# Kernel tuning notes

Hardware: AMD Instinct MI355X
Metric: run time of the kernel (lower is better)

The kernel has to match this reference:

```python
import jax, jax.numpy as jnp
import numpy as np

HIDDEN = 128
VOCAB = 100000
NUM_CLASSES = 5
N_LEAVES = 65536  # complete binary tree -> 2*N_LEAVES-1 = 131071 nodes


def setup_inputs() -> dict:
    key = jax.random.key(0)
    ks = jax.random.split(key, 24)
    H, C = HIDDEN, NUM_CLASSES

    def w(k, o, i):
        return (jax.random.normal(k, (o, i), jnp.float32) / np.sqrt(i)).astype(jnp.float32)

    def b(k, o):
        return jax.random.normal(k, (o,), jnp.float32) * 0.01

    inp = {
        "leaf_tokens": jax.random.randint(ks[0], (N_LEAVES,), 0, VOCAB, dtype=jnp.int64 if jax.config.jax_enable_x64 else jnp.int32).astype(jnp.int32),
        "node_labels": jax.random.randint(ks[1], (2 * N_LEAVES - 1,), 0, NUM_CLASSES).astype(jnp.int32),
        "embed": jax.random.uniform(ks[2], (VOCAB, H), jnp.float32, -0.5 / H, 0.5 / H),
        "W_i_w": w(ks[3], H, H), "W_i_b": b(ks[4], H),
        "W_o_w": w(ks[5], H, H), "W_o_b": b(ks[6], H),
        "W_u_w": w(ks[7], H, H), "W_u_b": b(ks[8], H),
        "U_i_w": w(ks[9], H, 2 * H), "U_i_b": b(ks[10], H),
        "U_o_w": w(ks[11], H, 2 * H), "U_o_b": b(ks[12], H),
        "U_u_w": w(ks[13], H, 2 * H), "U_u_b": b(ks[14], H),
        "F1_w": w(ks[15], H, H), "F1_b": b(ks[16], H),
        "F2_w": w(ks[17], H, H), "F2_b": b(ks[18], H),
        "out_w": w(ks[19], C, H), "out_b": b(ks[20], C),
    }
    return inp


def reference(leaf_tokens, node_labels, embed,
              W_i_w, W_i_b, W_o_w, W_o_b, W_u_w, W_u_b,
              U_i_w, U_i_b, U_o_w, U_o_b, U_u_w, U_u_b,
              F1_w, F1_b, F2_w, F2_b, out_w, out_b):
    def aff(x, wgt, bias):
        return x @ wgt.T + bias

    # ---- leaves: x = embed[token]; c = sigmoid(W_i x) * tanh(W_u x) ----
    x = embed[leaf_tokens]                          # [L, H]
    i = jax.nn.sigmoid(aff(x, W_i_w, W_i_b))
    o = jax.nn.sigmoid(aff(x, W_o_w, W_o_b))
    u = jnp.tanh(aff(x, W_u_w, W_u_b))
    c = i * u
    h = o * jnp.tanh(c)
    outs = [aff(h, out_w, out_b)]                   # dropout is identity at eval

    # ---- internal levels, bottom-up, all same-depth nodes batched ----
    n_levels = int(np.log2(N_LEAVES))
    for _ in range(n_levels):
        hl, hr = h[0::2], h[1::2]                   # [n/2, H] each
        cl, cr = c[0::2], c[1::2]
        xc = jnp.concatenate([hl, hr], axis=1)      # [n/2, 2H]
        i = jax.nn.sigmoid(aff(xc, U_i_w, U_i_b))
        o = jax.nn.sigmoid(aff(xc, U_o_w, U_o_b))
        u = jnp.tanh(aff(xc, U_u_w, U_u_b))
        f1 = jax.nn.sigmoid(aff(hl, F1_w, F1_b))
        f2 = jax.nn.sigmoid(aff(hr, F2_w, F2_b))
        c = i * u + f1 * cl + f2 * cr
        h = o * jnp.tanh(c)
        outs.append(aff(h, out_w, out_b))

    outputs = jnp.concatenate(outs, axis=0)         # [2L-1, num_classes]
    return outputs, node_labels
```

## Files before the change

### kernel.cpp

```cpp
#include <hip/hip_runtime.h>
#include <hip/hip_bf16.h>
#include <math.h>

#define H    128
#define NC   5
#define LPI  264
#define LPL  136
#define HPAD 136
#define CBP  132

typedef unsigned short ushort_t;
using frag_ab = __attribute__((ext_vector_type(8))) short;
using frag_cd = __attribute__((ext_vector_type(4))) float;

__device__ __forceinline__ float fsig(float x) {
    return __builtin_amdgcn_rcpf(1.0f + __expf(-x));
}
__device__ __forceinline__ float ftanh_(float x) {
    float e = __expf(-2.0f * fabsf(x));
    float t = (1.0f - e) * __builtin_amdgcn_rcpf(1.0f + e);
    return copysignf(t, x);
}
__device__ __forceinline__ ushort_t f2bf(float f) {
    __hip_bfloat16 b = __float2bfloat16(f);
    return *reinterpret_cast<ushort_t*>(&b);
}

__global__ __launch_bounds__(256) void prep_weights(
    const float* __restrict__ Ui, const float* __restrict__ Uo, const float* __restrict__ Uu,
    const float* __restrict__ F1, const float* __restrict__ F2,
    const float* __restrict__ Wi, const float* __restrict__ Wo, const float* __restrict__ Wu,
    const float* __restrict__ Wout,
    ushort_t* __restrict__ Wf, ushort_t* __restrict__ Wlf, ushort_t* __restrict__ Woutf)
{
    int e = blockIdx.x * 256 + threadIdx.x;
    if (e < 131072) {
        int kc = e >> 12, rem = e & 4095;
        int n = rem >> 3, j7 = rem & 7;
        int k = kc * 8 + j7;
        int g = n >> 7, jc = n & 127;
        float v;
        if (g == 0)      v = Ui[jc * 256 + k];
        else if (g == 1) v = Uo[jc * 256 + k];
        else if (g == 2) v = Uu[jc * 256 + k];
        else             v = (k < 128) ? F1[jc * 128 + k] : F2[jc * 128 + k - 128];
        Wf[e] = f2bf(v);
    } else if (e < 180224) {
        int e2 = e - 131072;
        int kc = e2 / 3072, rem = e2 % 3072;
        int n = rem >> 3, j7 = rem & 7;
        int k = kc * 8 + j7;
        int g = n >> 7, jc = n & 127;
        float v = (g == 0) ? Wi[jc * 128 + k] : (g == 1) ? Wo[jc * 128 + k] : Wu[jc * 128 + k];
        Wlf[e2] = f2bf(v);
    } else {
        int e3 = e - 180224;
        int kcq = e3 >> 7, rem = e3 & 127;
        int col = rem >> 3, j7 = rem & 7;
        int k = kcq * 8 + j7;
        float v = (col < NC) ? Wout[col * H + k] : 0.0f;
        Woutf[e3] = f2bf(v);
    }
}

__global__ __launch_bounds__(512) void leaf_l1_mfma(
    const int* __restrict__ tokens, const float* __restrict__ embed,
    const ushort_t* __restrict__ Wlf, const ushort_t* __restrict__ Wf,
    const ushort_t* __restrict__ Woutf,
    const float* __restrict__ bi, const float* __restrict__ bo, const float* __restrict__ bu,
    const float* __restrict__ bui, const float* __restrict__ buo, const float* __restrict__ buu,
    const float* __restrict__ bf1, const float* __restrict__ bf2,
    const float* __restrict__ bout,
    const int* __restrict__ labels, float* __restrict__ lab_out,
    ushort_t* __restrict__ h1_out, float* __restrict__ c1_out,
    float* __restrict__ out_leaf, float* __restrict__ out_l1)
{
    __shared__ ushort_t xs [32 * LPL];
    __shared__ ushort_t hh [32 * HPAD];
    __shared__ ushort_t hh2[16 * HPAD];
    __shared__ float    cbL[32 * CBP];
    __shared__ ushort_t xs2[16 * LPI];
    const int tid = threadIdx.x;
    const int node_base  = blockIdx.x * 32;
    const int node1_base = blockIdx.x * 16;

    if (tid < 64) {
        int id = blockIdx.x * 64 + tid;
        if (id < 131071) lab_out[id] = (float)labels[id];
    }

    {
        int m = tid >> 4, kp = (tid & 15) * 8;
        const float* src = embed + (size_t)tokens[node_base + m] * H + kp;
        ushort_t tmp[8];
#pragma unroll
        for (int v = 0; v < 2; ++v) {
            float4 f = *(const float4*)(src + v * 4);
            tmp[v * 4 + 0] = f2bf(f.x); tmp[v * 4 + 1] = f2bf(f.y);
            tmp[v * 4 + 2] = f2bf(f.z); tmp[v * 4 + 3] = f2bf(f.w);
        }
        *(uint4*)&xs[m * LPL + kp] = *(uint4*)tmp;
    }

    const int w = tid >> 6, lane = tid & 63;
    const int mA = lane & 15, q = lane >> 4, nlane = lane & 15;

    frag_ab wb[4];
#pragma unroll
    for (int kc8 = 0; kc8 < 4; ++kc8)
        wb[kc8] = *(const frag_ab*)&Woutf[(((kc8 * 4 + q) * 16) + nlane) * 8];
    float bout_l = (nlane < NC) ? bout[nlane] : 0.0f;

    const int jt = w;
    const int j = jt * 16 + nlane;
    __syncthreads();

    frag_ab a[2][4];
#pragma unroll
    for (int t = 0; t < 2; ++t)
#pragma unroll
        for (int kc8 = 0; kc8 < 4; ++kc8)
            a[t][kc8] = *(const frag_ab*)&xs[(t * 16 + mA) * LPL + (kc8 * 4 + q) * 8];

    {
        frag_cd acc[3][2];
#pragma unroll
        for (int g = 0; g < 3; ++g)
#pragma unroll
            for (int t = 0; t < 2; ++t) acc[g][t] = (frag_cd){0.f, 0.f, 0.f, 0.f};
#pragma unroll
        for (int kc8 = 0; kc8 < 4; ++kc8) {
            int kcq = kc8 * 4 + q;
            const ushort_t* wp = &Wlf[((size_t)kcq * 384 + jt * 16 + nlane) * 8];
#pragma unroll
            for (int g = 0; g < 3; ++g) {
                frag_ab b = *(const frag_ab*)(wp + (size_t)g * H * 8);
                acc[g][0] = __builtin_amdgcn_mfma_f32_16x16x32_bf16(a[0][kc8], b, acc[g][0], 0, 0, 0);
                acc[g][1] = __builtin_amdgcn_mfma_f32_16x16x32_bf16(a[1][kc8], b, acc[g][1], 0, 0, 0);
            }
        }
        float bi_ = bi[j], bo_ = bo[j], bu_ = bu[j];
#pragma unroll
        for (int t = 0; t < 2; ++t)
#pragma unroll
            for (int r = 0; r < 4; ++r) {
                int nloc = t * 16 + q * 4 + r;
                float i_ = fsig(acc[0][t][r] + bi_);
                float o_ = fsig(acc[1][t][r] + bo_);
                float u_ = ftanh_(acc[2][t][r] + bu_);
                float c_ = i_ * u_;
                float h_ = o_ * ftanh_(c_);
                cbL[nloc * CBP + j] = c_;
                ushort_t hb = f2bf(h_);
                hh[nloc * HPAD + j] = hb;
                xs2[(nloc >> 1) * LPI + (nloc & 1) * H + j] = hb;
            }
    }
    __syncthreads();

    frag_ab a1[8];
#pragma unroll
    for (int kc8 = 0; kc8 < 8; ++kc8)
        a1[kc8] = *(const frag_ab*)&xs2[mA * LPI + (kc8 * 4 + q) * 8];

    if (w < 2) {
        frag_cd ha = (frag_cd){0.f, 0.f, 0.f, 0.f};
#pragma unroll
        for (int kc8 = 0; kc8 < 4; ++kc8) {
            frag_ab av = *(const frag_ab*)&hh[(w * 16 + mA) * HPAD + (kc8 * 4 + q) * 8];
            ha = __builtin_amdgcn_mfma_f32_16x16x32_bf16(av, wb[kc8], ha, 0, 0, 0);
        }
        if (nlane < NC) {
#pragma unroll
            for (int r = 0; r < 4; ++r)
                out_leaf[(size_t)(node_base + w * 16 + q * 4 + r) * NC + nlane] = ha[r] + bout_l;
        }
    }

    {
        frag_cd acc[5];
#pragma unroll
        for (int g = 0; g < 5; ++g) acc[g] = (frag_cd){0.f, 0.f, 0.f, 0.f};
#pragma unroll
        for (int kc8 = 0; kc8 < 8; ++kc8) {
            int kcq = kc8 * 4 + q;
            const ushort_t* wp = &Wf[((size_t)kcq * 512 + jt * 16 + nlane) * 8];
#pragma unroll
            for (int g = 0; g < 4; ++g) {
                frag_ab b = *(const frag_ab*)(wp + (size_t)g * H * 8);
                int gi = (g < 3) ? g : (kc8 < 4 ? 3 : 4);
                acc[gi] = __builtin_amdgcn_mfma_f32_16x16x32_bf16(a1[kc8], b, acc[gi], 0, 0, 0);
            }
        }
        float bi_ = bui[j], bo_ = buo[j], bu_ = buu[j], b1_ = bf1[j], b2_ = bf2[j];
#pragma unroll
        for (int r = 0; r < 4; ++r) {
            int nloc = q * 4 + r;
            int nd = node1_base + nloc;
            float i_  = fsig(acc[0][r] + bi_);
            float o_  = fsig(acc[1][r] + bo_);
            float u_  = ftanh_(acc[2][r] + bu_);
            float f1_ = fsig(acc[3][r] + b1_);
            float f2_ = fsig(acc[4][r] + b2_);
            float cl = cbL[(2 * nloc) * CBP + j];
            float cr = cbL[(2 * nloc + 1) * CBP + j];
            float c_ = fmaf(i_, u_, fmaf(f1_, cl, f2_ * cr));
            float h_ = o_ * ftanh_(c_);
            c1_out[(size_t)nd * H + j] = c_;
            ushort_t hb = f2bf(h_);
            h1_out[(size_t)nd * H + j] = hb;
            hh2[nloc * HPAD + j] = hb;
        }
    }
    __syncthreads();

    if (w == 0) {
        frag_cd ha = (frag_cd){0.f, 0.f, 0.f, 0.f};
#pragma unroll
        for (int kc8 = 0; kc8 < 4; ++kc8) {
            frag_ab av = *(const frag_ab*)&hh2[mA * HPAD + (kc8 * 4 + q) * 8];
            ha = __builtin_amdgcn_mfma_f32_16x16x32_bf16(av, wb[kc8], ha, 0, 0, 0);
        }
        if (nlane < NC) {
#pragma unroll
            for (int r = 0; r < 4; ++r)
                out_l1[(size_t)(node1_base + q * 4 + r) * NC + nlane] = ha[r] + bout_l;
        }
    }
}

__global__ __launch_bounds__(512) void subtree_mfma(
    const ushort_t* __restrict__ h_prev, const float* __restrict__ c_prev,
    const ushort_t* __restrict__ Wf, const ushort_t* __restrict__ Woutf,
    const float* __restrict__ bui, const float* __restrict__ buo, const float* __restrict__ buu,
    const float* __restrict__ bf1, const float* __restrict__ bf2,
    const float* __restrict__ bout,
    ushort_t* __restrict__ h_out, float* __restrict__ c_out,
    float* __restrict__ out_base)
{
    __shared__ ushort_t xsA[32 * LPI];
    __shared__ ushort_t xsB[16 * LPI];
    __shared__ float    cbA[32 * CBP];
    __shared__ float    cbB[16 * CBP];
    __shared__ ushort_t hh [32 * HPAD];
    const int tid = threadIdx.x;
    const int NB  = gridDim.x;

    {
        int m = tid >> 4, kp = (tid & 15) * 16;
        const uint4* s = (const uint4*)(h_prev +
            ((size_t)2 * (blockIdx.x * 32 + m) + (kp >> 7)) * H + (kp & 127));
        uint4* d = (uint4*)&xsA[m * LPI + kp];
        d[0] = s[0]; d[1] = s[1];
    }

    const int w = tid >> 6, lane = tid & 63;
    const int mA = lane & 15, q = lane >> 4, nlane = lane & 15;

    frag_ab wb[4];
#pragma unroll
    for (int kc8 = 0; kc8 < 4; ++kc8)
        wb[kc8] = *(const frag_ab*)&Woutf[(((kc8 * 4 + q) * 16) + nlane) * 8];
    float bout_l = (nlane < NC) ? bout[nlane] : 0.0f;

    const int jt = w;
    const int j = jt * 16 + nlane;
    const float bi_ = bui[j], bo_ = buo[j], bu_ = buu[j], b1_ = bf1[j], b2_ = bf2[j];

    size_t out_off = 0;
    for (int lev = 0; lev < 4; ++lev) {
        const int N = 32 >> lev;
        const int ntiles = (N + 15) >> 4;
        const int gbase = blockIdx.x * N;
        ushort_t* xs_cur = (lev & 1) ? xsB : xsA;
        ushort_t* xs_nxt = (lev & 1) ? xsA : xsB;
        float*    cb_out = (lev & 1) ? cbB : cbA;
        const float* cb_in = (lev & 1) ? cbA : cbB;
        __syncthreads();

        for (int t = 0; t < ntiles; ++t) {
            frag_cd acc[5];
#pragma unroll
            for (int g = 0; g < 5; ++g) acc[g] = (frag_cd){0.f, 0.f, 0.f, 0.f};
#pragma unroll
            for (int kc8 = 0; kc8 < 8; ++kc8) {
                int kcq = kc8 * 4 + q;
                frag_ab av = *(const frag_ab*)&xs_cur[(t * 16 + mA) * LPI + kcq * 8];
                const ushort_t* wp = &Wf[((size_t)kcq * 512 + jt * 16 + nlane) * 8];
#pragma unroll
                for (int g = 0; g < 4; ++g) {
                    frag_ab b = *(const frag_ab*)(wp + (size_t)g * H * 8);
                    int gi = (g < 3) ? g : (kc8 < 4 ? 3 : 4);
                    acc[gi] = __builtin_amdgcn_mfma_f32_16x16x32_bf16(av, b, acc[gi], 0, 0, 0);
                }
            }
#pragma unroll
            for (int r = 0; r < 4; ++r) {
                int nloc = t * 16 + q * 4 + r;
                if (nloc < N) {
                    float i_  = fsig(acc[0][r] + bi_);
                    float o_  = fsig(acc[1][r] + bo_);
                    float u_  = ftanh_(acc[2][r] + bu_);
                    float f1_ = fsig(acc[3][r] + b1_);
                    float f2_ = fsig(acc[4][r] + b2_);
                    float cl, cr;
                    if (lev == 0) {
                        cl = c_prev[((size_t)2 * (gbase + nloc)) * H + j];
                        cr = c_prev[((size_t)2 * (gbase + nloc) + 1) * H + j];
                    } else {
                        cl = cb_in[(2 * nloc) * CBP + j];
                        cr = cb_in[(2 * nloc + 1) * CBP + j];
                    }
                    float c_ = fmaf(i_, u_, fmaf(f1_, cl, f2_ * cr));
                    float h_ = o_ * ftanh_(c_);
                    ushort_t hb = f2bf(h_);
                    hh[nloc * HPAD + j] = hb;
                    if (lev < 3) {
                        cb_out[nloc * CBP + j] = c_;
                        xs_nxt[(nloc >> 1) * LPI + (nloc & 1) * H + j] = hb;
                    } else {
                        c_out[(size_t)(gbase + nloc) * H + j] = c_;
                        h_out[(size_t)(gbase + nloc) * H + j] = hb;
                    }
                }
            }
        }
        __syncthreads();
        if (w < ntiles) {
            frag_cd ha = (frag_cd){0.f, 0.f, 0.f, 0.f};
#pragma unroll
            for (int kc8 = 0; kc8 < 4; ++kc8) {
                frag_ab av = *(const frag_ab*)&hh[(w * 16 + mA) * HPAD + (kc8 * 4 + q) * 8];
                ha = __builtin_amdgcn_mfma_f32_16x16x32_bf16(av, wb[kc8], ha, 0, 0, 0);
            }
            if (nlane < NC) {
#pragma unroll
                for (int r = 0; r < 4; ++r) {
                    int nd = w * 16 + q * 4 + r;
                    if (nd < N)
                        out_base[out_off + (size_t)(gbase + nd) * NC + nlane] = ha[r] + bout_l;
                }
            }
        }
        out_off += (size_t)NB * N * NC;
    }
}

__global__ __launch_bounds__(512) void tail_mfma(
    const ushort_t* __restrict__ h_prev, const float* __restrict__ c_prev,
    const ushort_t* __restrict__ Wf, const ushort_t* __restrict__ Woutf,
    const float* __restrict__ bui, const float* __restrict__ buo, const float* __restrict__ buu,
    const float* __restrict__ bf1, const float* __restrict__ bf2,
    const float* __restrict__ bout, float* __restrict__ out)
{
    __shared__ ushort_t xsA[64 * LPI];
    __shared__ ushort_t xsB[32 * LPI];
    __shared__ float    cbA[64 * H];
    __shared__ float    cbB[32 * H];
    __shared__ ushort_t hh[64 * HPAD];
    const int tid = threadIdx.x;
    const int w = tid >> 6, lane = tid & 63;
    const int mA = lane & 15, q = lane >> 4, nlane = lane & 15;

    {
        int m = tid >> 3, kp = (tid & 7) * 32;
        const uint4* s = (const uint4*)(h_prev + ((size_t)2 * m + (kp >> 7)) * H + (kp & 127));
        uint4* d = (uint4*)&xsA[m * LPI + kp];
#pragma unroll
        for (int i = 0; i < 4; ++i) d[i] = s[i];
    }

    frag_ab wb[4];
#pragma unroll
    for (int kc8 = 0; kc8 < 4; ++kc8)
        wb[kc8] = *(const frag_ab*)&Woutf[(((kc8 * 4 + q) * 16) + nlane) * 8];
    float bout_l = (nlane < NC) ? bout[nlane] : 0.0f;

    const int jt = w;
    const int j = jt * 16 + nlane;
    const float bi_ = bui[j], bo_ = buo[j], bu_ = buu[j], b1_ = bf1[j], b2_ = bf2[j];

    float* outp = out;
    for (int lev = 0; lev < 7; ++lev) {
        const int N = 64 >> lev;
        const int ntiles = (N + 15) >> 4;
        ushort_t* xs_cur = (lev & 1) ? xsB : xsA;
        ushort_t* xs_nxt = (lev & 1) ? xsA : xsB;
        float*    cb_out = (lev & 1) ? cbB : cbA;
        const float* cb_in = (lev & 1) ? cbA : cbB;
        __syncthreads();

        for (int t = 0; t < ntiles; ++t) {
            frag_cd acc[5];
#pragma unroll
            for (int g = 0; g < 5; ++g) acc[g] = (frag_cd){0.f, 0.f, 0.f, 0.f};
#pragma unroll
            for (int kc8 = 0; kc8 < 8; ++kc8) {
                int kcq = kc8 * 4 + q;
                frag_ab av = *(const frag_ab*)&xs_cur[(t * 16 + mA) * LPI + kcq * 8];
                const ushort_t* wp = &Wf[((size_t)kcq * 512 + jt * 16 + nlane) * 8];
#pragma unroll
                for (int g = 0; g < 4; ++g) {
                    frag_ab b = *(const frag_ab*)(wp + (size_t)g * H * 8);
                    int gi = (g < 3) ? g : (kc8 < 4 ? 3 : 4);
                    acc[gi] = __builtin_amdgcn_mfma_f32_16x16x32_bf16(av, b, acc[gi], 0, 0, 0);
                }
            }
#pragma unroll
            for (int r = 0; r < 4; ++r) {
                int nloc = t * 16 + q * 4 + r;
                if (nloc < N) {
                    float i_  = fsig(acc[0][r] + bi_);
                    float o_  = fsig(acc[1][r] + bo_);
                    float u_  = ftanh_(acc[2][r] + bu_);
                    float f1_ = fsig(acc[3][r] + b1_);
                    float f2_ = fsig(acc[4][r] + b2_);
                    float cl, cr;
                    if (lev == 0) {
                        cl = c_prev[((size_t)2 * nloc) * H + j];
                        cr = c_prev[((size_t)2 * nloc + 1) * H + j];
                    } else {
                        cl = cb_in[(2 * nloc) * H + j];
                        cr = cb_in[(2 * nloc + 1) * H + j];
                    }
                    float c_ = fmaf(i_, u_, fmaf(f1_, cl, f2_ * cr));
                    float h_ = o_ * ftanh_(c_);
                    cb_out[nloc * H + j] = c_;
                    ushort_t hb = f2bf(h_);
                    hh[nloc * HPAD + j] = hb;
                    xs_nxt[(nloc >> 1) * LPI + (nloc & 1) * H + j] = hb;
                }
            }
        }
        __syncthreads();
        if (w < ntiles) {
            frag_cd ha = (frag_cd){0.f, 0.f, 0.f, 0.f};
#pragma unroll
            for (int kc8 = 0; kc8 < 4; ++kc8) {
                frag_ab av = *(const frag_ab*)&hh[(w * 16 + mA) * HPAD + (kc8 * 4 + q) * 8];
                ha = __builtin_amdgcn_mfma_f32_16x16x32_bf16(av, wb[kc8], ha, 0, 0, 0);
            }
            if (nlane < NC) {
#pragma unroll
                for (int r = 0; r < 4; ++r) {
                    int nd = w * 16 + q * 4 + r;
                    if (nd < N) outp[(size_t)nd * NC + nlane] = ha[r] + bout_l;
                }
            }
        }
        outp += (size_t)N * NC;
    }
}

extern "C" void kernel_launch(void* const* d_in, const int* in_sizes, int n_in,
                              void* d_out, int out_size, void* d_ws, size_t ws_size,
                              hipStream_t stream)
{
    const int*   tokens = (const int*)d_in[0];
    const int*   labels = (const int*)d_in[1];
    const float* embed  = (const float*)d_in[2];
    const float* Wi = (const float*)d_in[3];  const float* bi  = (const float*)d_in[4];
    const float* Wo = (const float*)d_in[5];  const float* bo  = (const float*)d_in[6];
    const float* Wu = (const float*)d_in[7];  const float* bu  = (const float*)d_in[8];
    const float* Ui = (const float*)d_in[9];  const float* bui = (const float*)d_in[10];
    const float* Uo = (const float*)d_in[11]; const float* buo = (const float*)d_in[12];
    const float* Uu = (const float*)d_in[13]; const float* buu = (const float*)d_in[14];
    const float* F1 = (const float*)d_in[15]; const float* bf1 = (const float*)d_in[16];
    const float* F2 = (const float*)d_in[17]; const float* bf2 = (const float*)d_in[18];
    const float* Wout = (const float*)d_in[19]; const float* bout = (const float*)d_in[20];
    float* out = (float*)d_out;

    const int NL = 65536;
    char* base = (char*)d_ws;
    ushort_t* Wf    = (ushort_t*)(base);
    ushort_t* Wlf   = (ushort_t*)(base + 327680);
    ushort_t* Woutf = (ushort_t*)(base + 425984);
    ushort_t* hA    = (ushort_t*)(base + 430080);
    ushort_t* hB    = (ushort_t*)(base + 17207296);
    float*    cA    = (float*)   (base + 25595904);
    float*    cB    = (float*)   (base + 59150336);

    prep_weights<<<712, 256, 0, stream>>>(Ui, Uo, Uu, F1, F2, Wi, Wo, Wu, Wout,
                                          Wf, Wlf, Woutf);

    const size_t totalN = 2 * (size_t)NL - 1;
    float* lab_out = out + totalN * NC;

    leaf_l1_mfma<<<NL / 32, 512, 0, stream>>>(
        tokens, embed, Wlf, Wf, Woutf, bi, bo, bu, bui, buo, buu, bf1, bf2,
        bout, labels, lab_out, hB, cB, out, out + (size_t)NL * NC);

    size_t off = (size_t)(NL + NL / 2) * NC;

    subtree_mfma<<<512, 512, 0, stream>>>(
        hB, cB, Wf, Woutf, bui, buo, buu, bf1, bf2, bout, hA, cA, out + off);
    off += (size_t)(16384 + 8192 + 4096 + 2048) * NC;

    subtree_mfma<<<32, 512, 0, stream>>>(
        hA, cA, Wf, Woutf, bui, buo, buu, bf1, bf2, bout, hB, cB, out + off);
    off += (size_t)(1024 + 512 + 256 + 128) * NC;

    tail_mfma<<<1, 512, 0, stream>>>(hB, cB, Wf, Woutf, bui, buo, buu, bf1, bf2,
                                     bout, out + off);
}
```

Measured before the change: 228.7 us.

## Shrink subtree blocks to 16 rows and shift levels from tail kernel

The subtree kernel now handles 16 nodes per block instead of 32, and is templated on level count. The first launch uses twice as many blocks (1024) and the second covers five levels with 64 blocks, so the single-block tail kernel starts from 32 nodes and runs six levels instead of seven. The aim is more parallelism in the mid-tree kernels and less serial work in the one-block tail. The cost is that the subtree kernels now do much of their per-level compute with partially filled 16-row MFMA tiles.

```diff
diff --git a/kernel.cpp b/kernel.cpp
--- a/kernel.cpp
+++ b/kernel.cpp
@@ -229,7 +229,8 @@
     }
 }
 
-__global__ __launch_bounds__(512) void subtree_mfma(
+template<int LEVELS>
+__global__ __launch_bounds__(512) void subtree16_mfma(
     const ushort_t* __restrict__ h_prev, const float* __restrict__ c_prev,
     const ushort_t* __restrict__ Wf, const ushort_t* __restrict__ Woutf,
     const float* __restrict__ bui, const float* __restrict__ buo, const float* __restrict__ buu,
@@ -238,20 +239,19 @@
     ushort_t* __restrict__ h_out, float* __restrict__ c_out,
     float* __restrict__ out_base)
 {
-    __shared__ ushort_t xsA[32 * LPI];
-    __shared__ ushort_t xsB[16 * LPI];
-    __shared__ float    cbA[32 * CBP];
-    __shared__ float    cbB[16 * CBP];
-    __shared__ ushort_t hh [32 * HPAD];
+    __shared__ ushort_t xsA[16 * LPI];
+    __shared__ ushort_t xsB[8  * LPI];
+    __shared__ float    cbA[16 * CBP];
+    __shared__ float    cbB[8  * CBP];
+    __shared__ ushort_t hh [16 * HPAD];
     const int tid = threadIdx.x;
     const int NB  = gridDim.x;
 
     {
-        int m = tid >> 4, kp = (tid & 15) * 16;
+        int m = tid >> 5, kp = (tid & 31) * 8;
         const uint4* s = (const uint4*)(h_prev +
-            ((size_t)2 * (blockIdx.x * 32 + m) + (kp >> 7)) * H + (kp & 127));
-        uint4* d = (uint4*)&xsA[m * LPI + kp];
-        d[0] = s[0]; d[1] = s[1];
+            ((size_t)2 * (blockIdx.x * 16 + m) + (kp >> 7)) * H + (kp & 127));
+        *(uint4*)&xsA[m * LPI + kp] = s[0];
     }
 
     const int w = tid >> 6, lane = tid & 63;
@@ -268,9 +268,9 @@
     const float bi_ = bui[j], bo_ = buo[j], bu_ = buu[j], b1_ = bf1[j], b2_ = bf2[j];
 
     size_t out_off = 0;
-    for (int lev = 0; lev < 4; ++lev) {
-        const int N = 32 >> lev;
-        const int ntiles = (N + 15) >> 4;
+#pragma unroll 1
+    for (int lev = 0; lev < LEVELS; ++lev) {
+        const int N = 16 >> lev;
         const int gbase = blockIdx.x * N;
         ushort_t* xs_cur = (lev & 1) ? xsB : xsA;
         ushort_t* xs_nxt = (lev & 1) ? xsA : xsB;
@@ -278,14 +278,14 @@
         const float* cb_in = (lev & 1) ? cbA : cbB;
         __syncthreads();
 
-        for (int t = 0; t < ntiles; ++t) {
+        {
             frag_cd acc[5];
 #pragma unroll
             for (int g = 0; g < 5; ++g) acc[g] = (frag_cd){0.f, 0.f, 0.f, 0.f};
 #pragma unroll
             for (int kc8 = 0; kc8 < 8; ++kc8) {
                 int kcq = kc8 * 4 + q;
-                frag_ab av = *(const frag_ab*)&xs_cur[(t * 16 + mA) * LPI + kcq * 8];
+                frag_ab av = *(const frag_ab*)&xs_cur[mA * LPI + kcq * 8];
                 const ushort_t* wp = &Wf[((size_t)kcq * 512 + jt * 16 + nlane) * 8];
 #pragma unroll
                 for (int g = 0; g < 4; ++g) {
@@ -296,7 +296,7 @@
             }
 #pragma unroll
             for (int r = 0; r < 4; ++r) {
-                int nloc = t * 16 + q * 4 + r;
+                int nloc = q * 4 + r;
                 if (nloc < N) {
                     float i_  = fsig(acc[0][r] + bi_);
                     float o_  = fsig(acc[1][r] + bo_);
@@ -315,7 +315,7 @@
                     float h_ = o_ * ftanh_(c_);
                     ushort_t hb = f2bf(h_);
                     hh[nloc * HPAD + j] = hb;
-                    if (lev < 3) {
+                    if (lev < LEVELS - 1) {
                         cb_out[nloc * CBP + j] = c_;
                         xs_nxt[(nloc >> 1) * LPI + (nloc & 1) * H + j] = hb;
                     } else {
@@ -326,17 +326,17 @@
             }
         }
         __syncthreads();
-        if (w < ntiles) {
+        if (w == 0) {
             frag_cd ha = (frag_cd){0.f, 0.f, 0.f, 0.f};
 #pragma unroll
             for (int kc8 = 0; kc8 < 4; ++kc8) {
-                frag_ab av = *(const frag_ab*)&hh[(w * 16 + mA) * HPAD + (kc8 * 4 + q) * 8];
+                frag_ab av = *(const frag_ab*)&hh[(mA) * HPAD + (kc8 * 4 + q) * 8];
                 ha = __builtin_amdgcn_mfma_f32_16x16x32_bf16(av, wb[kc8], ha, 0, 0, 0);
             }
             if (nlane < NC) {
 #pragma unroll
                 for (int r = 0; r < 4; ++r) {
-                    int nd = w * 16 + q * 4 + r;
+                    int nd = q * 4 + r;
                     if (nd < N)
                         out_base[out_off + (size_t)(gbase + nd) * NC + nlane] = ha[r] + bout_l;
                 }
@@ -353,21 +353,20 @@
     const float* __restrict__ bf1, const float* __restrict__ bf2,
     const float* __restrict__ bout, float* __restrict__ out)
 {
-    __shared__ ushort_t xsA[64 * LPI];
-    __shared__ ushort_t xsB[32 * LPI];
-    __shared__ float    cbA[64 * H];
-    __shared__ float    cbB[32 * H];
-    __shared__ ushort_t hh[64 * HPAD];
+    __shared__ ushort_t xsA[32 * LPI];
+    __shared__ ushort_t xsB[16 * LPI];
+    __shared__ float    cbA[32 * H];
+    __shared__ float    cbB[16 * H];
+    __shared__ ushort_t hh[32 * HPAD];
     const int tid = threadIdx.x;
     const int w = tid >> 6, lane = tid & 63;
     const int mA = lane & 15, q = lane >> 4, nlane = lane & 15;
 
     {
-        int m = tid >> 3, kp = (tid & 7) * 32;
+        int m = tid >> 4, kp = (tid & 15) * 16;
         const uint4* s = (const uint4*)(h_prev + ((size_t)2 * m + (kp >> 7)) * H + (kp & 127));
         uint4* d = (uint4*)&xsA[m * LPI + kp];
-#pragma unroll
-        for (int i = 0; i < 4; ++i) d[i] = s[i];
+        d[0] = s[0]; d[1] = s[1];
     }
 
     frag_ab wb[4];
@@ -381,8 +380,9 @@
     const float bi_ = bui[j], bo_ = buo[j], bu_ = buu[j], b1_ = bf1[j], b2_ = bf2[j];
 
     float* outp = out;
-    for (int lev = 0; lev < 7; ++lev) {
-        const int N = 64 >> lev;
+#pragma unroll 1
+    for (int lev = 0; lev < 6; ++lev) {
+        const int N = 32 >> lev;
         const int ntiles = (N + 15) >> 4;
         ushort_t* xs_cur = (lev & 1) ? xsB : xsA;
         ushort_t* xs_nxt = (lev & 1) ? xsA : xsB;
@@ -490,16 +490,14 @@
         tokens, embed, Wlf, Wf, Woutf, bi, bo, bu, bui, buo, buu, bf1, bf2,
         bout, labels, lab_out, hB, cB, out, out + (size_t)NL * NC);
 
-    size_t off = (size_t)(NL + NL / 2) * NC;
-
-    subtree_mfma<<<512, 512, 0, stream>>>(
-        hB, cB, Wf, Woutf, bui, buo, buu, bf1, bf2, bout, hA, cA, out + off);
-    off += (size_t)(16384 + 8192 + 4096 + 2048) * NC;
-
-    subtree_mfma<<<32, 512, 0, stream>>>(
-        hA, cA, Wf, Woutf, bui, buo, buu, bf1, bf2, bout, hB, cB, out + off);
-    off += (size_t)(1024 + 512 + 256 + 128) * NC;
+    subtree16_mfma<4><<<1024, 512, 0, stream>>>(
+        hB, cB, Wf, Woutf, bui, buo, buu, bf1, bf2, bout, hA, cA,
+        out + (size_t)98304 * NC);
+
+    subtree16_mfma<5><<<64, 512, 0, stream>>>(
+        hA, cA, Wf, Woutf, bui, buo, buu, bf1, bf2, bout, hB, cB,
+        out + (size_t)129024 * NC);
 
     tail_mfma<<<1, 512, 0, stream>>>(hB, cB, Wf, Woutf, bui, buo, buu, bf1, bf2,
-                                     bout, out + off);
-}
+                                     bout, out + (size_t)131008 * NC);
+}
```

After: 233.4 us. 2.1% more time.
